# Performance work log

Hardware: AMD Instinct MI355X
Metric: run time of the kernel (lower is better)

Reference implementation:

```python
import jax, jax.numpy as jnp
import numpy as np

EPS = 1e-6

def _rms_norm(x, w):
    # normalize over last dim (head_dim)
    var = jnp.mean(jnp.square(x), axis=-1, keepdims=True)
    return x * jax.lax.rsqrt(var + EPS) * w

def _rotate_half(x):
    half = x.shape[-1] // 2
    first, second = x[..., :half], x[..., half:]
    return jnp.concatenate([-second, first], axis=-1)

def _apply_rope(x, cos, sin):
    # x: [B,H,S,D]; cos/sin: [B,S,D] -> broadcast over heads
    return x * cos[:, None] + _rotate_half(x) * sin[:, None]

def setup_inputs() -> dict:
    key = jax.random.key(0)
    ks = jax.random.split(key, 10)
    B, Sq, Sk, Dm, H = 2, 2048, 2048, 2048, 16
    hd = Dm // H
    scale = 1.0 / np.sqrt(Dm)
    return {
        "x": jax.random.normal(ks[0], (B, Sq, Dm), jnp.float32),
        "context": jax.random.normal(ks[1], (B, Sk, Dm), jnp.float32),
        "cos_q": jax.random.uniform(ks[2], (B, Sq, hd), jnp.float32),
        "sin_q": jax.random.uniform(ks[3], (B, Sq, hd), jnp.float32),
        "cos_k": jax.random.uniform(ks[4], (B, Sk, hd), jnp.float32),
        "sin_k": jax.random.uniform(ks[5], (B, Sk, hd), jnp.float32),
        "Wq": jax.random.normal(ks[6], (Dm, Dm), jnp.float32) * scale,
        "Wk": jax.random.normal(ks[7], (Dm, Dm), jnp.float32) * scale,
        "Wv": jax.random.normal(ks[8], (Dm, Dm), jnp.float32) * scale,
        "Wo": jax.random.normal(ks[9], (Dm, Dm), jnp.float32) * scale,
        "q_norm_w": jnp.ones((hd,), jnp.float32),
        "k_norm_w": jnp.ones((hd,), jnp.float32),
    }

def reference(x, context, cos_q, sin_q, cos_k, sin_k, Wq, Wk, Wv, Wo, q_norm_w, k_norm_w):
    B, Sq, Dm = x.shape
    hd = q_norm_w.shape[0]
    H = Dm // hd
    # projections (torch Linear: y = x @ W.T), reshape to [B,H,S,D]
    q = (x @ Wq.T).reshape(B, Sq, H, hd).transpose(0, 2, 1, 3)
    k = (context @ Wk.T).reshape(B, -1, H, hd).transpose(0, 2, 1, 3)
    v = (context @ Wv.T).reshape(B, -1, H, hd).transpose(0, 2, 1, 3)
    # per-head QK RMSNorm
    q = _rms_norm(q, q_norm_w)
    k = _rms_norm(k, k_norm_w)
    # RoPE
    q = _apply_rope(q, cos_q, sin_q)
    k = _apply_rope(k, cos_k, sin_k)
    # SDPA, scale = 1/sqrt(head_dim)
    scale = 1.0 / np.sqrt(hd).astype(np.float32)
    scores = jnp.einsum('bhqd,bhkd->bhqk', q, k) * scale
    attn = jax.nn.softmax(scores, axis=-1)
    y = jnp.einsum('bhqk,bhkd->bhqd', attn, v)
    y = y.transpose(0, 2, 1, 3).reshape(B, Sq, Dm)
    return y @ Wo.T
```

## Files before the change

kernel.cpp:

```cpp
#include <hip/hip_runtime.h>


typedef __attribute__((ext_vector_type(8))) short bf16x8;
typedef __attribute__((ext_vector_type(4))) float f32x4;

#define AS1(p) ((__attribute__((address_space(1))) void*)(p))
#define AS3(p) ((__attribute__((address_space(3))) void*)(p))
#define STG(g, l) __builtin_amdgcn_global_load_lds(AS1(g), AS3(l), 16, 0, 0)

__device__ __forceinline__ unsigned short f2bf(float f) {
  unsigned int u = __float_as_uint(f);
  u += 0x7fffu + ((u >> 16) & 1u);
  return (unsigned short)(u >> 16);
}
__device__ __forceinline__ float bf2f(unsigned short u) {
  return __uint_as_float(((unsigned int)u) << 16);
}

constexpr int B_ = 2, S_ = 2048, DM = 2048, H_ = 16, HD = 128;
constexpr int M_ = B_ * S_;

__global__ __launch_bounds__(256) void castbf(const float* __restrict__ X,
                                              unsigned short* __restrict__ Y, int n4) {
  int i = blockIdx.x * 256 + threadIdx.x;
  if (i >= n4) return;
  float4 v = ((const float4*)X)[i];
  ushort4 u;
  u.x = f2bf(v.x); u.y = f2bf(v.y); u.z = f2bf(v.z); u.w = f2bf(v.w);
  ((ushort4*)Y)[i] = u;
}

template <int BF16OUT>
__device__ __forceinline__ void gemm_core(const unsigned short* __restrict__ A,
                                          const unsigned short* __restrict__ Bw,
                                          void* __restrict__ Cv,
                                          unsigned short* lds) {
  const int tid = threadIdx.x, wave = tid >> 6, lane = tid & 63;
  const int quad = lane >> 4, l16 = lane & 15;
  const int m0 = blockIdx.x * 128, n0 = blockIdx.y * 256;
  const int wn = wave * 64;
  constexpr int NT = DM / 32;
  constexpr int SLOT = 12288;

  f32x4 acc[8][4];
#pragma unroll
  for (int f = 0; f < 8; f++)
#pragma unroll
    for (int g = 0; g < 4; g++) acc[f][g] = (f32x4){0.f, 0.f, 0.f, 0.f};

  const unsigned short* srcA[2];
  const unsigned short* srcB[4];
#pragma unroll
  for (int i = 0; i < 2; i++) {
    int c = tid + i * 256, L = c >> 3, ph = c & 7, j = ph ^ (L & 7);
    srcA[i] = A + (size_t)(m0 + L + ((j >> 2) << 6)) * DM + (j & 3) * 8;
  }
#pragma unroll
  for (int i = 0; i < 4; i++) {
    int c = tid + i * 256, L = c >> 3, ph = c & 7, j = ph ^ (L & 7);
    srcB[i] = Bw + (size_t)(n0 + L + ((j >> 2) << 7)) * DM + (j & 3) * 8;
  }

#define STAGEK(T, S)                                                           \
  { const int ko = (T) << 5; unsigned short* lb = lds + (S) * SLOT + wave * 512;\
    STG(srcA[0] + ko, lb);                                                     \
    STG(srcA[1] + ko, lb + 2048);                                              \
    STG(srcB[0] + ko, lb + 4096);                                              \
    STG(srcB[1] + ko, lb + 6144);                                              \
    STG(srcB[2] + ko, lb + 8192);                                              \
    STG(srcB[3] + ko, lb + 10240); }

  const int x8 = l16 & 7;
  const int ab0 = l16 * 64 + ((quad ^ x8)) * 8;
  const int ab1 = l16 * 64 + (((4 | quad) ^ x8)) * 8;
  const int bb  = 4096 + (wn & 64) * 64 + l16 * 64 +
                  ((((wave >> 1) << 2) | quad) ^ x8) * 8;

  STAGEK(0, 0) STAGEK(1, 1)
  asm volatile("s_waitcnt vmcnt(6)" ::: "memory");
  __builtin_amdgcn_s_barrier();

  int st = 0, s2 = 2;
  for (int t = 0; t < NT; ++t) {
    const unsigned short* ls = lds + st * SLOT;
    bf16x8 af[8], bfv[4];
#pragma unroll
    for (int f = 0; f < 4; f++) af[f]     = *(const bf16x8*)(ls + f * 1024 + ab0);
#pragma unroll
    for (int f = 0; f < 4; f++) af[f + 4] = *(const bf16x8*)(ls + f * 1024 + ab1);
#pragma unroll
    for (int g = 0; g < 4; g++) bfv[g]    = *(const bf16x8*)(ls + g * 1024 + bb);

    if (t + 2 < NT) STAGEK(t + 2, s2)
    if (t < NT - 2)       asm volatile("s_waitcnt vmcnt(6)" ::: "memory");
    else if (t == NT - 2) asm volatile("s_waitcnt vmcnt(0)" ::: "memory");
    if (t < NT - 1) __builtin_amdgcn_s_barrier();

    __builtin_amdgcn_s_setprio(1);
#pragma unroll
    for (int f = 0; f < 8; f++)
#pragma unroll
      for (int g = 0; g < 4; g++)
        acc[f][g] = __builtin_amdgcn_mfma_f32_16x16x32_bf16(af[f], bfv[g], acc[f][g], 0, 0, 0);
    __builtin_amdgcn_s_setprio(0);

    st++; if (st == 3) st = 0;
    s2++; if (s2 == 3) s2 = 0;
  }
#undef STAGEK

#pragma unroll
  for (int f = 0; f < 8; f++)
#pragma unroll
    for (int g = 0; g < 4; g++) {
      const size_t row = (size_t)(m0 + f * 16 + quad * 4);
      const int col = n0 + wn + g * 16 + l16;
      if (BF16OUT) {
        unsigned short* cp = (unsigned short*)Cv + row * DM + col;
#pragma unroll
        for (int r = 0; r < 4; r++) cp[(size_t)r * DM] = f2bf(acc[f][g][r]);
      } else {
        float* cp = (float*)Cv + row * DM + col;
#pragma unroll
        for (int r = 0; r < 4; r++) cp[(size_t)r * DM] = acc[f][g][r];
      }
    }
}

__global__ __launch_bounds__(256, 2) void gemm_qkv(const unsigned short* __restrict__ xb,
                                                   const unsigned short* __restrict__ cb,
                                                   const unsigned short* __restrict__ Wq,
                                                   const unsigned short* __restrict__ Wk,
                                                   const unsigned short* __restrict__ Wv,
                                                   unsigned short* __restrict__ Pq,
                                                   unsigned short* __restrict__ Pk,
                                                   unsigned short* __restrict__ Pv) {
  __shared__ __align__(16) unsigned short lds[3 * 12288];
  const int z = blockIdx.z;
  const unsigned short* A  = (z == 0) ? xb : cb;
  const unsigned short* Bw = (z == 0) ? Wq : (z == 1) ? Wk : Wv;
  unsigned short* C        = (z == 0) ? Pq : (z == 1) ? Pk : Pv;
  gemm_core<1>(A, Bw, C, lds);
}

__global__ __launch_bounds__(256, 2) void gemm_bt(const unsigned short* __restrict__ A,
                                                  const unsigned short* __restrict__ Bw,
                                                  float* __restrict__ C) {
  __shared__ __align__(16) unsigned short lds[3 * 12288];
  gemm_core<0>(A, Bw, C, lds);
}

__global__ __launch_bounds__(256) void normrope(const unsigned short* __restrict__ X,
                                                const float* __restrict__ Cs,
                                                const float* __restrict__ Sn,
                                                const float* __restrict__ W,
                                                unsigned short* __restrict__ Out,
                                                float scale) {
  int gw = (blockIdx.x * 256 + threadIdx.x) >> 6;
  int lane = threadIdx.x & 63;
  int h = gw & 15, bs = gw >> 4;
  int s = bs & (S_ - 1), b = bs >> 11;
  const unsigned short* xr = X + (size_t)gw * HD;
  float x0 = bf2f(xr[lane]), x1 = bf2f(xr[lane + 64]);
  float ss = x0 * x0 + x1 * x1;
#pragma unroll
  for (int off = 32; off > 0; off >>= 1) ss += __shfl_xor(ss, off);
  float rr = rsqrtf(ss * (1.0f / 128.0f) + 1e-6f);
  float n0 = x0 * rr * W[lane], n1 = x1 * rr * W[lane + 64];
  const float* cp = Cs + (size_t)bs * HD;
  const float* sp = Sn + (size_t)bs * HD;
  float o0 = (n0 * cp[lane] - n1 * sp[lane]) * scale;
  float o1 = (n1 * cp[lane + 64] + n0 * sp[lane + 64]) * scale;
  unsigned short* orow = Out + (((size_t)(b * H_ + h)) * S_ + s) * HD;
  orow[lane] = f2bf(o0);
  orow[lane + 64] = f2bf(o1);
}

__global__ __launch_bounds__(256) void vtrans(const unsigned short* __restrict__ Vf,
                                              unsigned short* __restrict__ Vt) {
  __shared__ unsigned short tile[128 * 72];
  const int tid = threadIdx.x;
  const int sc = blockIdx.x & 31;
  const int bh = blockIdx.x >> 5;
  const int b = bh >> 4, h = bh & 15;
  const int s0 = sc * 64;
#pragma unroll
  for (int it = 0; it < 4; ++it) {
    int ci = it * 256 + tid;
    int s = ci >> 4, dc = ci & 15;
    bf16x8 v = *(const bf16x8*)(Vf + ((size_t)(b * S_ + s0 + s)) * DM + h * HD + dc * 8);
    unsigned short* tp = tile + (dc * 8) * 72 + s;
#pragma unroll
    for (int e = 0; e < 8; e++) tp[e * 72] = (unsigned short)v[e];
  }
  __syncthreads();
#pragma unroll
  for (int it = 0; it < 4; ++it) {
    int cj = it * 256 + tid;
    int d = cj >> 3, scx = cj & 7;
    bf16x8 vv = *(const bf16x8*)(tile + d * 72 + scx * 8);
    *(bf16x8*)(Vt + ((size_t)bh * HD + d) * S_ + s0 + scx * 8) = vv;
  }
}

__global__ __launch_bounds__(256, 2) void flash(const unsigned short* __restrict__ Q,
                                                const unsigned short* __restrict__ Kt,
                                                const unsigned short* __restrict__ Vt,
                                                unsigned short* __restrict__ Y) {
  __shared__ unsigned short lK[2 * 64 * HD];
  __shared__ unsigned short lV[2 * HD * 64];
  __shared__ unsigned short lP[4 * 1024];
  const int tid = threadIdx.x, wave = tid >> 6, lane = tid & 63;
  const int quad = lane >> 4, l16 = lane & 15;
  const int qb = blockIdx.x & 15;
  const int bh = blockIdx.x >> 4;
  const int b = bh >> 4, h = bh & 15;
  const int q0 = qb * 128 + wave * 32;

  bf16x8 aq[2][4];
#pragma unroll
  for (int u = 0; u < 2; u++) {
    const unsigned short* qrow = Q + ((size_t)bh * S_ + q0 + u * 16 + l16) * HD;
#pragma unroll
    for (int t = 0; t < 4; t++) aq[u][t] = *(const bf16x8*)(qrow + t * 32 + quad * 8);
  }
  f32x4 o[2][8];
#pragma unroll
  for (int u = 0; u < 2; u++)
#pragma unroll
    for (int t = 0; t < 8; t++) o[u][t] = (f32x4){0.f, 0.f, 0.f, 0.f};
  float lsum[2][4] = {{0.f, 0.f, 0.f, 0.f}, {0.f, 0.f, 0.f, 0.f}};

  const unsigned short* kbase = Kt + (size_t)bh * S_ * HD;
  const unsigned short* vbase = Vt + (size_t)bh * HD * S_;
  unsigned short* lPw = lP + wave * 1024;
  const int mrow = quad * 4;
  const int xsl = (l16 >> 1) & 3;
  const int xsl7 = (l16 >> 1) & 7;

#define STAGEKV(K0, BUF)                                                       \
  {                                                                            \
    const unsigned short* kb_ = kbase + (size_t)(K0) * HD;                     \
    const unsigned short* vb_ = vbase + (K0);                                  \
    _Pragma("unroll")                                                          \
    for (int call = 0; call < 4; ++call) {                                     \
      int c = call * 256 + tid;                         \
      int key = c >> 4, sk = c & 15;           \
      int dck = sk ^ (key & 15);                                               \
      STG(kb_ + (size_t)key * HD + dck * 8,                                    \
          lK + (BUF) * 8192 + (call * 256 + wave * 64) * 8);                   \
      int dv = c >> 3, sv = c & 7;             \
      int kc = sv ^ ((dv >> 1) & 7);                                           \
      STG(vb_ + (size_t)dv * S_ + kc * 8,                                      \
          lV + (BUF) * 8192 + (call * 256 + wave * 64) * 8);                   \
    }                                                                          \
  }

  STAGEKV(0, 0)

  for (int it = 0; it < S_ / 64; ++it) {
    if (it + 1 < S_ / 64) {
      STAGEKV((it + 1) * 64, (it + 1) & 1)
      asm volatile("s_waitcnt vmcnt(8)" ::: "memory");
    } else {
      asm volatile("s_waitcnt vmcnt(0)" ::: "memory");
    }
    __builtin_amdgcn_s_barrier();

    const unsigned short* lKc = lK + (it & 1) * 8192;
    const unsigned short* lVc = lV + (it & 1) * 8192;

#pragma unroll
    for (int h2 = 0; h2 < 2; ++h2) {
      f32x4 s0[2] = {(f32x4){0.f, 0.f, 0.f, 0.f}, (f32x4){0.f, 0.f, 0.f, 0.f}};
      f32x4 s1[2] = {(f32x4){0.f, 0.f, 0.f, 0.f}, (f32x4){0.f, 0.f, 0.f, 0.f}};
      {
        const unsigned short* krow0 = lKc + (h2 * 32 + l16) * HD;
        const unsigned short* krow1 = krow0 + 16 * HD;
        __builtin_amdgcn_s_setprio(1);
#pragma unroll
        for (int t = 0; t < 4; t++) {
          int dcq = t * 4 + quad;
          bf16x8 kf0 = *(const bf16x8*)(krow0 + (dcq ^ l16) * 8);
          bf16x8 kf1 = *(const bf16x8*)(krow1 + (dcq ^ l16) * 8);
#pragma unroll
          for (int u = 0; u < 2; u++) {
            s0[u] = __builtin_amdgcn_mfma_f32_16x16x32_bf16(aq[u][t], kf0, s0[u], 0, 0, 0);
            s1[u] = __builtin_amdgcn_mfma_f32_16x16x32_bf16(aq[u][t], kf1, s1[u], 0, 0, 0);
          }
        }
        __builtin_amdgcn_s_setprio(0);
      }
#pragma unroll
      for (int u = 0; u < 2; u++) {
        unsigned short* lPu = lPw + u * 512;
#pragma unroll
        for (int r = 0; r < 4; r++) {
          int m = mrow + r;
          int sx = (m >> 1) & 3;
          float p0 = __expf(s0[u][r]);
          float p1 = __expf(s1[u][r]);
          lsum[u][r] += p0 + p1;
          int kc0 = l16 >> 3;
          lPu[m * 32 + ((kc0 ^ sx)) * 8 + (l16 & 7)] = f2bf(p0);
          lPu[m * 32 + (((kc0 + 2) ^ sx)) * 8 + (l16 & 7)] = f2bf(p1);
        }
      }
      bf16x8 pf[2];
#pragma unroll
      for (int u = 0; u < 2; u++)
        pf[u] = *(const bf16x8*)(lPw + u * 512 + l16 * 32 + (quad ^ xsl) * 8);
      __builtin_amdgcn_s_setprio(1);
#pragma unroll
      for (int t = 0; t < 8; t++) {
        bf16x8 vf = *(const bf16x8*)(lVc + (t * 16 + l16) * 64 + ((h2 * 4 + quad) ^ xsl7) * 8);
#pragma unroll
        for (int u = 0; u < 2; u++)
          o[u][t] = __builtin_amdgcn_mfma_f32_16x16x32_bf16(pf[u], vf, o[u][t], 0, 0, 0);
      }
      __builtin_amdgcn_s_setprio(0);
    }

    __builtin_amdgcn_s_barrier();
  }
#undef STAGEKV

#pragma unroll
  for (int off = 1; off < 16; off <<= 1) {
#pragma unroll
    for (int u = 0; u < 2; u++)
#pragma unroll
      for (int r = 0; r < 4; r++) lsum[u][r] += __shfl_xor(lsum[u][r], off);
  }
  float inv[2][4];
#pragma unroll
  for (int u = 0; u < 2; u++)
#pragma unroll
    for (int r = 0; r < 4; r++) inv[u][r] = 1.0f / lsum[u][r];
#pragma unroll
  for (int u = 0; u < 2; u++)
#pragma unroll
    for (int t = 0; t < 8; t++)
#pragma unroll
      for (int r = 0; r < 4; r++) {
        size_t idx = ((size_t)b * S_ + q0 + u * 16 + mrow + r) * DM + h * HD + t * 16 + l16;
        Y[idx] = f2bf(o[u][t][r] * inv[u][r]);
      }
}

extern "C" void kernel_launch(void* const* d_in, const int* in_sizes, int n_in,
                              void* d_out, int out_size, void* d_ws, size_t ws_size,
                              hipStream_t stream) {
  const float* x    = (const float*)d_in[0];
  const float* ctx  = (const float*)d_in[1];
  const float* cosq = (const float*)d_in[2];
  const float* sinq = (const float*)d_in[3];
  const float* cosk = (const float*)d_in[4];
  const float* sink = (const float*)d_in[5];
  const float* Wq   = (const float*)d_in[6];
  const float* Wk   = (const float*)d_in[7];
  const float* Wv   = (const float*)d_in[8];
  const float* Wo   = (const float*)d_in[9];
  const float* qw   = (const float*)d_in[10];
  const float* kw   = (const float*)d_in[11];

  char* ws = (char*)d_ws;
  const size_t ACT2 = (size_t)M_ * DM * 2;
  const size_t W2   = (size_t)DM * DM * 2;
  unsigned short* xb  = (unsigned short*)(ws);
  unsigned short* cb  = (unsigned short*)(ws + ACT2);
  unsigned short* Wqb = (unsigned short*)(ws + 2 * ACT2);
  unsigned short* Wkb = (unsigned short*)(ws + 2 * ACT2 + W2);
  unsigned short* Wvb = (unsigned short*)(ws + 2 * ACT2 + 2 * W2);
  unsigned short* Wob = (unsigned short*)(ws + 2 * ACT2 + 3 * W2);
  unsigned short* Pq  = (unsigned short*)(ws + 2 * ACT2 + 4 * W2);
  unsigned short* Pk  = (unsigned short*)(ws + 3 * ACT2 + 4 * W2);
  unsigned short* Pv  = (unsigned short*)(ws + 4 * ACT2 + 4 * W2);
  unsigned short* qn = xb;
  unsigned short* kn = Wqb;
  unsigned short* vt = cb;
  unsigned short* yb = Pq;

  const float scale = 0.0883883476483184f;

  castbf<<<M_ * DM / 1024, 256, 0, stream>>>(x, xb, M_ * DM / 4);
  castbf<<<M_ * DM / 1024, 256, 0, stream>>>(ctx, cb, M_ * DM / 4);
  castbf<<<DM * DM / 1024, 256, 0, stream>>>(Wq, Wqb, DM * DM / 4);
  castbf<<<DM * DM / 1024, 256, 0, stream>>>(Wk, Wkb, DM * DM / 4);
  castbf<<<DM * DM / 1024, 256, 0, stream>>>(Wv, Wvb, DM * DM / 4);
  castbf<<<DM * DM / 1024, 256, 0, stream>>>(Wo, Wob, DM * DM / 4);

  dim3 gq(M_ / 128, DM / 256, 3);
  gemm_qkv<<<gq, 256, 0, stream>>>(xb, cb, Wqb, Wkb, Wvb, Pq, Pk, Pv);

  normrope<<<M_ * H_ / 4, 256, 0, stream>>>(Pq, cosq, sinq, qw, qn, scale);
  normrope<<<M_ * H_ / 4, 256, 0, stream>>>(Pk, cosk, sink, kw, kn, 1.0f);
  vtrans<<<B_ * H_ * (S_ / 64), 256, 0, stream>>>(Pv, vt);

  flash<<<B_ * H_ * (S_ / 128), 256, 0, stream>>>(qn, kn, vt, yb);

  dim3 gg(M_ / 128, DM / 256);
  gemm_bt<<<gg, 256, 0, stream>>>(yb, Wob, (float*)d_out);

  (void)in_sizes; (void)n_in; (void)out_size; (void)ws_size;
}
```

Baseline: 457.4 us.

## Split GEMM k-step into two half-phases interleaving LDS reads, staging, and MFMAs

Restructures the projection GEMM main loop so each k-step runs as two halves. Each half loads part of the A fragments from LDS, issues half of the global-to-LDS prefetch for step t+2, then runs half of the MFMA block, with extra barriers between phases. The goal is to spread LDS reads and memory issue more evenly across compute and shrink register pressure from holding all eight A fragments at once. The extra barriers per iteration add synchronization cost and may reduce overlap between waves.

```diff
diff --git a/kernel.cpp b/kernel.cpp
--- a/kernel.cpp
+++ b/kernel.cpp
@@ -61,11 +61,13 @@
     srcB[i] = Bw + (size_t)(n0 + L + ((j >> 2) << 7)) * DM + (j & 3) * 8;
   }
 
-#define STAGEK(T, S)                                                           \
+#define STAGE_H0(T, S)                                                         \
   { const int ko = (T) << 5; unsigned short* lb = lds + (S) * SLOT + wave * 512;\
     STG(srcA[0] + ko, lb);                                                     \
     STG(srcA[1] + ko, lb + 2048);                                              \
-    STG(srcB[0] + ko, lb + 4096);                                              \
+    STG(srcB[0] + ko, lb + 4096); }
+#define STAGE_H1(T, S)                                                         \
+  { const int ko = (T) << 5; unsigned short* lb = lds + (S) * SLOT + wave * 512;\
     STG(srcB[1] + ko, lb + 6144);                                              \
     STG(srcB[2] + ko, lb + 8192);                                              \
     STG(srcB[3] + ko, lb + 10240); }
@@ -76,38 +78,52 @@
   const int bb  = 4096 + (wn & 64) * 64 + l16 * 64 +
                   ((((wave >> 1) << 2) | quad) ^ x8) * 8;
 
-  STAGEK(0, 0) STAGEK(1, 1)
+  STAGE_H0(0, 0) STAGE_H1(0, 0)
+  STAGE_H0(1, 1) STAGE_H1(1, 1)
   asm volatile("s_waitcnt vmcnt(6)" ::: "memory");
   __builtin_amdgcn_s_barrier();
 
   int st = 0, s2 = 2;
   for (int t = 0; t < NT; ++t) {
     const unsigned short* ls = lds + st * SLOT;
-    bf16x8 af[8], bfv[4];
-#pragma unroll
-    for (int f = 0; f < 4; f++) af[f]     = *(const bf16x8*)(ls + f * 1024 + ab0);
-#pragma unroll
-    for (int f = 0; f < 4; f++) af[f + 4] = *(const bf16x8*)(ls + f * 1024 + ab1);
-#pragma unroll
-    for (int g = 0; g < 4; g++) bfv[g]    = *(const bf16x8*)(ls + g * 1024 + bb);
-
-    if (t + 2 < NT) STAGEK(t + 2, s2)
+
+    bf16x8 af0[4], bfv[4];
+#pragma unroll
+    for (int f = 0; f < 4; f++) af0[f] = *(const bf16x8*)(ls + f * 1024 + ab0);
+#pragma unroll
+    for (int g = 0; g < 4; g++) bfv[g] = *(const bf16x8*)(ls + g * 1024 + bb);
+    if (t + 2 < NT) STAGE_H0(t + 2, s2)
+    __builtin_amdgcn_s_barrier();
+    __builtin_amdgcn_s_setprio(1);
+#pragma unroll
+    for (int f = 0; f < 4; f++)
+#pragma unroll
+      for (int g = 0; g < 4; g++)
+        acc[f][g] = __builtin_amdgcn_mfma_f32_16x16x32_bf16(af0[f], bfv[g], acc[f][g], 0, 0, 0);
+    __builtin_amdgcn_s_setprio(0);
+    __builtin_amdgcn_s_barrier();
+
+    bf16x8 af1[4];
+#pragma unroll
+    for (int f = 0; f < 4; f++) af1[f] = *(const bf16x8*)(ls + f * 1024 + ab1);
+    if (t + 2 < NT) STAGE_H1(t + 2, s2)
     if (t < NT - 2)       asm volatile("s_waitcnt vmcnt(6)" ::: "memory");
     else if (t == NT - 2) asm volatile("s_waitcnt vmcnt(0)" ::: "memory");
+    __builtin_amdgcn_s_barrier();
+    __builtin_amdgcn_s_setprio(1);
+#pragma unroll
+    for (int f = 0; f < 4; f++)
+#pragma unroll
+      for (int g = 0; g < 4; g++)
+        acc[f + 4][g] = __builtin_amdgcn_mfma_f32_16x16x32_bf16(af1[f], bfv[g], acc[f + 4][g], 0, 0, 0);
+    __builtin_amdgcn_s_setprio(0);
     if (t < NT - 1) __builtin_amdgcn_s_barrier();
-
-    __builtin_amdgcn_s_setprio(1);
-#pragma unroll
-    for (int f = 0; f < 8; f++)
-#pragma unroll
-      for (int g = 0; g < 4; g++)
-        acc[f][g] = __builtin_amdgcn_mfma_f32_16x16x32_bf16(af[f], bfv[g], acc[f][g], 0, 0, 0);
-    __builtin_amdgcn_s_setprio(0);
 
     st++; if (st == 3) st = 0;
     s2++; if (s2 == 3) s2 = 0;
   }
-#undef STAGEK
+#undef STAGE_H0
+#undef STAGE_H1
 
 #pragma unroll
   for (int f = 0; f < 8; f++)
```

Measured after the change: 455.8 us. Within noise of the previous version (-0.4%).
